# Kernel tuning notes

Measured on AMD Instinct MI355X. Metric: run time of the kernel, lower is better.

Reference implementation:

```python
import jax, jax.numpy as jnp
import numpy as np


def setup_inputs() -> dict:
    key = jax.random.key(0)
    k_x, k_W, k_b, k_ids, k_w = jax.random.split(key, 5)
    N_ADAPTERS, D_OUT, D_IN = 32, 1024, 1024
    B, S = 2, 2048
    K = 8  # number of active adapters
    x = jax.random.normal(k_x, (B, S, D_IN), dtype=jnp.float32)
    W = jax.random.normal(k_W, (N_ADAPTERS, D_OUT, D_IN), dtype=jnp.float32)
    b = jax.random.normal(k_b, (N_ADAPTERS, D_OUT), dtype=jnp.float32)
    ids = jax.random.randint(k_ids, (K,), 0, N_ADAPTERS, dtype=jnp.int64)
    weights = jax.random.uniform(k_w, (K,), dtype=jnp.float32)
    return {"x": x, "W": W, "b": b, "ids": ids, "weights": weights}


def reference(x, W, b, ids, weights):
    # Original: out_i = Linear_{ids[i]}(x); output = sum_i weights[i] * out_i
    Wsel = W[ids]  # [k, o, d]  gather of selected adapter weights
    bsel = b[ids]  # [k, o]
    # Fused weighted mixture of k small GEMMs (same math as loop + weighted sum)
    out = jnp.einsum("k,kod,bsd->bso", weights, Wsel, x)
    out = out + jnp.einsum("k,ko->o", weights, bsel)
    return out
```

## Files before the change

### kernel.cpp

```cpp
#include <hip/hip_runtime.h>
#include <hip/hip_bf16.h>
#include <stdint.h>


typedef __attribute__((ext_vector_type(8))) short short8;
typedef __attribute__((ext_vector_type(4))) float float4v;

#define DIMK 1024
#define DIMN 1024
#define DIMM 4096

__device__ __forceinline__ unsigned short f2bf_rtn(float f) {
  union { float f; unsigned u; } v; v.f = f;
  unsigned u = v.u;
  return (unsigned short)((u + 0x7fffu + ((u >> 16) & 1u)) >> 16);
}

__global__ __launch_bounds__(256) void prep_kernel(
    const float* __restrict__ x, const float* __restrict__ W,
    const float* __restrict__ bia, const int* __restrict__ ids,
    const float* __restrict__ wts,
    unsigned short* __restrict__ xb, unsigned short* __restrict__ Wc,
    float* __restrict__ bc, int K)
{
  const int bid = blockIdx.x;
  if (bid < 1024) {
    const int t  = bid * 256 + threadIdx.x;
    const int o  = t >> 8;
    const int d4 = (t & 255) << 2;
    float ax = 0.f, ay = 0.f, az = 0.f, aw = 0.f;
    for (int k = 0; k < K; ++k) {
      const float wk = wts[k];
      const float4 w4 = *reinterpret_cast<const float4*>(
          &W[((size_t)ids[k] << 20) + ((size_t)o << 10) + d4]);
      ax += wk * w4.x; ay += wk * w4.y; az += wk * w4.z; aw += wk * w4.w;
    }
    ushort4 r;
    r.x = f2bf_rtn(ax); r.y = f2bf_rtn(ay); r.z = f2bf_rtn(az); r.w = f2bf_rtn(aw);
    *reinterpret_cast<ushort4*>(&Wc[(size_t)t << 2]) = r;
    if (t < DIMN) {
      float s = 0.f;
      for (int k = 0; k < K; ++k) s += wts[k] * bia[ids[k] * DIMN + t];
      bc[t] = s;
    }
  } else {
    const size_t t = (size_t)(bid - 1024) * 256 + threadIdx.x;
    const float4 v = *reinterpret_cast<const float4*>(&x[t << 2]);
    ushort4 r;
    r.x = f2bf_rtn(v.x); r.y = f2bf_rtn(v.y); r.z = f2bf_rtn(v.z); r.w = f2bf_rtn(v.w);
    *reinterpret_cast<ushort4*>(&xb[t << 2]) = r;
  }
}

__device__ __forceinline__ void load_lds16(const void* g, void* l) {
  __builtin_amdgcn_global_load_lds(
      (const __attribute__((address_space(1))) void*)g,
      (__attribute__((address_space(3))) void*)l, 16, 0, 0);
}

__global__ __launch_bounds__(256, 2) void gemm_kernel(
    const unsigned short* __restrict__ xb,
    const unsigned short* __restrict__ Wc,
    const float* __restrict__ bc,
    float* __restrict__ out)
{
  constexpr int BK = 64;
  __shared__ __align__(16) unsigned short As[64 * BK];
  __shared__ __align__(16) unsigned short Bs[128 * BK];

  const int tid  = threadIdx.x;
  const int wave = tid >> 6;
  const int lane = tid & 63;
  const int m0 = blockIdx.y * 64;
  const int n0 = blockIdx.x * 128;

  const int srow = lane >> 3;
  const int scol = (((lane & 7) ^ srow) << 3);
  const unsigned short* gA0 = xb + (size_t)(m0 + wave * 16 + srow) * DIMK + scol;
  const unsigned short* gA1 = gA0 + 8 * DIMK;
  const unsigned short* gB0 = Wc + (size_t)(n0 + wave * 32 + srow) * DIMK + scol;
  const unsigned short* gB1 = gB0 + 8 * DIMK;
  const unsigned short* gB2 = gB0 + 16 * DIMK;
  const unsigned short* gB3 = gB0 + 24 * DIMK;
  unsigned short* lA0 = &As[wave * 16 * BK];
  unsigned short* lA1 = lA0 + 8 * BK;
  unsigned short* lB0 = &Bs[wave * 32 * BK];
  unsigned short* lB1 = lB0 + 8 * BK;
  unsigned short* lB2 = lB0 + 16 * BK;
  unsigned short* lB3 = lB0 + 24 * BK;

  const int wm   = (wave >> 1) * 32;
  const int wn   = (wave & 1) * 64;
  const int quad = lane >> 4;
  const int r16  = lane & 15;
  const int rx   = r16 & 7;
  const int po0  = ((quad ^ rx) << 3);
  const int po1  = (((4 + quad) ^ rx) << 3);

  const float4v zero = {0.f, 0.f, 0.f, 0.f};
  float4v acc[2][4];
#pragma unroll
  for (int i = 0; i < 2; ++i)
#pragma unroll
    for (int j = 0; j < 4; ++j) acc[i][j] = zero;

  for (int k0 = 0; k0 < DIMK; k0 += BK) {
    load_lds16(gA0 + k0, lA0);
    load_lds16(gA1 + k0, lA1);
    load_lds16(gB0 + k0, lB0);
    load_lds16(gB1 + k0, lB1);
    load_lds16(gB2 + k0, lB2);
    load_lds16(gB3 + k0, lB3);
    __syncthreads();

#pragma unroll
    for (int s = 0; s < 2; ++s) {
      const int po = s ? po1 : po0;
      short8 af[2], bf[4];
#pragma unroll
      for (int mt = 0; mt < 2; ++mt)
        af[mt] = *reinterpret_cast<const short8*>(&As[(wm + mt * 16 + r16) * BK + po]);
#pragma unroll
      for (int nt = 0; nt < 4; ++nt)
        bf[nt] = *reinterpret_cast<const short8*>(&Bs[(wn + nt * 16 + r16) * BK + po]);
#pragma unroll
      for (int mt = 0; mt < 2; ++mt)
#pragma unroll
        for (int nt = 0; nt < 4; ++nt)
          acc[mt][nt] = __builtin_amdgcn_mfma_f32_16x16x32_bf16(af[mt], bf[nt], acc[mt][nt], 0, 0, 0);
    }
    __syncthreads();
  }

#pragma unroll
  for (int nt = 0; nt < 4; ++nt) {
    const int col = n0 + wn + nt * 16 + r16;
    const float bias = bc[col];
#pragma unroll
    for (int mt = 0; mt < 2; ++mt) {
      const int rbase = m0 + wm + mt * 16 + quad * 4;
#pragma unroll
      for (int r = 0; r < 4; ++r)
        out[(size_t)(rbase + r) * DIMN + col] = acc[mt][nt][r] + bias;
    }
  }
}

extern "C" void kernel_launch(void* const* d_in, const int* in_sizes, int n_in,
                              void* d_out, int out_size, void* d_ws, size_t ws_size,
                              hipStream_t stream) {
  const float* x   = (const float*)d_in[0];
  const float* W   = (const float*)d_in[1];
  const float* b   = (const float*)d_in[2];
  const int*   ids = (const int*)d_in[3];
  const float* wts = (const float*)d_in[4];
  float* out = (float*)d_out;
  const int K = in_sizes[3];

  unsigned short* xb = (unsigned short*)d_ws;
  unsigned short* Wc = (unsigned short*)((char*)d_ws + (8u << 20));
  float*          bc = (float*)((char*)d_ws + (10u << 20));

  prep_kernel<<<5120, 256, 0, stream>>>(x, W, b, ids, wts, xb, Wc, bc, K);
  dim3 grid(DIMN / 128, DIMM / 64);
  gemm_kernel<<<grid, 256, 0, stream>>>(xb, Wc, bc, out);
}
```

Before: 201.9 us.

## Double-buffer GEMM LDS tiles and unroll adapter mixing in prep kernel

The GEMM kernel now uses two LDS buffers per operand, so the asynchronous global-to-LDS loads for the next K tile are issued before computing on the current tile. This aims to hide global load latency behind MFMA work. It doubles the kernel's LDS footprint, which may lower occupancy. The prep kernel also loads adapter ids and weights into registers once, fully unrolls the adapter loop for up to 8 adapters (silently ignoring any beyond 8), and converts two x vectors per thread with a smaller grid.

```diff
diff --git a/kernel.cpp b/kernel.cpp
--- a/kernel.cpp
+++ b/kernel.cpp
@@ -25,30 +25,41 @@
 {
   const int bid = blockIdx.x;
   if (bid < 1024) {
+    int   id[8];
+    float wv[8];
+#pragma unroll
+    for (int k = 0; k < 8; ++k) {
+      id[k] = (k < K) ? ids[k] : 0;
+      wv[k] = (k < K) ? wts[k] : 0.f;
+    }
     const int t  = bid * 256 + threadIdx.x;
     const int o  = t >> 8;
     const int d4 = (t & 255) << 2;
     float ax = 0.f, ay = 0.f, az = 0.f, aw = 0.f;
-    for (int k = 0; k < K; ++k) {
-      const float wk = wts[k];
+#pragma unroll
+    for (int k = 0; k < 8; ++k) {
       const float4 w4 = *reinterpret_cast<const float4*>(
-          &W[((size_t)ids[k] << 20) + ((size_t)o << 10) + d4]);
-      ax += wk * w4.x; ay += wk * w4.y; az += wk * w4.z; aw += wk * w4.w;
+          &W[((size_t)id[k] << 20) + ((size_t)o << 10) + d4]);
+      ax += wv[k] * w4.x; ay += wv[k] * w4.y; az += wv[k] * w4.z; aw += wv[k] * w4.w;
     }
     ushort4 r;
     r.x = f2bf_rtn(ax); r.y = f2bf_rtn(ay); r.z = f2bf_rtn(az); r.w = f2bf_rtn(aw);
     *reinterpret_cast<ushort4*>(&Wc[(size_t)t << 2]) = r;
     if (t < DIMN) {
       float s = 0.f;
-      for (int k = 0; k < K; ++k) s += wts[k] * bia[ids[k] * DIMN + t];
+#pragma unroll
+      for (int k = 0; k < 8; ++k) s += wv[k] * bia[id[k] * DIMN + t];
       bc[t] = s;
     }
   } else {
-    const size_t t = (size_t)(bid - 1024) * 256 + threadIdx.x;
-    const float4 v = *reinterpret_cast<const float4*>(&x[t << 2]);
-    ushort4 r;
-    r.x = f2bf_rtn(v.x); r.y = f2bf_rtn(v.y); r.z = f2bf_rtn(v.z); r.w = f2bf_rtn(v.w);
-    *reinterpret_cast<ushort4*>(&xb[t << 2]) = r;
+    const size_t t0 = (size_t)(bid - 1024) * 512 + threadIdx.x;
+    const float4 v0 = *reinterpret_cast<const float4*>(&x[t0 << 2]);
+    const float4 v1 = *reinterpret_cast<const float4*>(&x[(t0 + 256) << 2]);
+    ushort4 r0, r1;
+    r0.x = f2bf_rtn(v0.x); r0.y = f2bf_rtn(v0.y); r0.z = f2bf_rtn(v0.z); r0.w = f2bf_rtn(v0.w);
+    r1.x = f2bf_rtn(v1.x); r1.y = f2bf_rtn(v1.y); r1.z = f2bf_rtn(v1.z); r1.w = f2bf_rtn(v1.w);
+    *reinterpret_cast<ushort4*>(&xb[t0 << 2]) = r0;
+    *reinterpret_cast<ushort4*>(&xb[(t0 + 256) << 2]) = r1;
   }
 }
 
@@ -65,8 +76,8 @@
     float* __restrict__ out)
 {
   constexpr int BK = 64;
-  __shared__ __align__(16) unsigned short As[64 * BK];
-  __shared__ __align__(16) unsigned short Bs[128 * BK];
+  __shared__ __align__(16) unsigned short As[2][64 * BK];
+  __shared__ __align__(16) unsigned short Bs[2][128 * BK];
 
   const int tid  = threadIdx.x;
   const int wave = tid >> 6;
@@ -77,17 +88,9 @@
   const int srow = lane >> 3;
   const int scol = (((lane & 7) ^ srow) << 3);
   const unsigned short* gA0 = xb + (size_t)(m0 + wave * 16 + srow) * DIMK + scol;
-  const unsigned short* gA1 = gA0 + 8 * DIMK;
   const unsigned short* gB0 = Wc + (size_t)(n0 + wave * 32 + srow) * DIMK + scol;
-  const unsigned short* gB1 = gB0 + 8 * DIMK;
-  const unsigned short* gB2 = gB0 + 16 * DIMK;
-  const unsigned short* gB3 = gB0 + 24 * DIMK;
-  unsigned short* lA0 = &As[wave * 16 * BK];
-  unsigned short* lA1 = lA0 + 8 * BK;
-  unsigned short* lB0 = &Bs[wave * 32 * BK];
-  unsigned short* lB1 = lB0 + 8 * BK;
-  unsigned short* lB2 = lB0 + 16 * BK;
-  unsigned short* lB3 = lB0 + 24 * BK;
+  const int aoff = wave * 16 * BK;
+  const int boff = wave * 32 * BK;
 
   const int wm   = (wave >> 1) * 32;
   const int wn   = (wave & 1) * 64;
@@ -104,32 +107,42 @@
 #pragma unroll
     for (int j = 0; j < 4; ++j) acc[i][j] = zero;
 
-  for (int k0 = 0; k0 < DIMK; k0 += BK) {
-    load_lds16(gA0 + k0, lA0);
-    load_lds16(gA1 + k0, lA1);
-    load_lds16(gB0 + k0, lB0);
-    load_lds16(gB1 + k0, lB1);
-    load_lds16(gB2 + k0, lB2);
-    load_lds16(gB3 + k0, lB3);
-    __syncthreads();
+  auto issue = [&](int buf, int k0) {
+    load_lds16(gA0 + k0,            &As[buf][aoff]);
+    load_lds16(gA0 + k0 + 8 * DIMK, &As[buf][aoff + 8 * BK]);
+    load_lds16(gB0 + k0,            &Bs[buf][boff]);
+    load_lds16(gB0 + k0 + 8 * DIMK, &Bs[buf][boff + 8 * BK]);
+    load_lds16(gB0 + k0 + 16 * DIMK, &Bs[buf][boff + 16 * BK]);
+    load_lds16(gB0 + k0 + 24 * DIMK, &Bs[buf][boff + 24 * BK]);
+  };
 
+  auto compute = [&](int buf) {
 #pragma unroll
     for (int s = 0; s < 2; ++s) {
       const int po = s ? po1 : po0;
       short8 af[2], bf[4];
 #pragma unroll
       for (int mt = 0; mt < 2; ++mt)
-        af[mt] = *reinterpret_cast<const short8*>(&As[(wm + mt * 16 + r16) * BK + po]);
+        af[mt] = *reinterpret_cast<const short8*>(&As[buf][(wm + mt * 16 + r16) * BK + po]);
 #pragma unroll
       for (int nt = 0; nt < 4; ++nt)
-        bf[nt] = *reinterpret_cast<const short8*>(&Bs[(wn + nt * 16 + r16) * BK + po]);
+        bf[nt] = *reinterpret_cast<const short8*>(&Bs[buf][(wn + nt * 16 + r16) * BK + po]);
 #pragma unroll
       for (int mt = 0; mt < 2; ++mt)
 #pragma unroll
         for (int nt = 0; nt < 4; ++nt)
           acc[mt][nt] = __builtin_amdgcn_mfma_f32_16x16x32_bf16(af[mt], bf[nt], acc[mt][nt], 0, 0, 0);
     }
+  };
+
+  issue(0, 0);
+  for (int k0 = 0; k0 < DIMK; k0 += 2 * BK) {
     __syncthreads();
+    if (k0 + BK < DIMK) issue(1, k0 + BK);
+    compute(0);
+    __syncthreads();
+    if (k0 + 2 * BK < DIMK) issue(0, k0 + 2 * BK);
+    compute(1);
   }
 
 #pragma unroll
@@ -161,7 +174,7 @@
   unsigned short* Wc = (unsigned short*)((char*)d_ws + (8u << 20));
   float*          bc = (float*)((char*)d_ws + (10u << 20));
 
-  prep_kernel<<<5120, 256, 0, stream>>>(x, W, b, ids, wts, xb, Wc, bc, K);
+  prep_kernel<<<3072, 256, 0, stream>>>(x, W, b, ids, wts, xb, Wc, bc, K);
   dim3 grid(DIMN / 128, DIMM / 64);
   gemm_kernel<<<grid, 256, 0, stream>>>(xb, Wc, bc, out);
 }
```

Measured after the change: 203.8 us. About the same (+0.9%).
